# Optimization experiments

Measured on AMD Instinct MI355X. Metric: run time of the kernel, lower is better.

The kernel has to match this reference:

```python
import jax, jax.numpy as jnp
import numpy as np

N_NODES = 50000
N_EDGES = 1_600_000
HIDDEN = 128
BOND = 16


def setup_inputs() -> dict:
    key = jax.random.key(0)
    ks = jax.random.split(key, 6)
    h = jax.random.normal(ks[0], (N_NODES, HIDDEN), dtype=jnp.float32)
    edge_index = jax.random.randint(ks[1], (2, N_EDGES), 0, N_NODES, dtype=jnp.int32)
    bond_features = jax.random.normal(ks[2], (N_EDGES, BOND), dtype=jnp.float32)
    fan_in1 = 2 * HIDDEN + BOND
    W1 = jax.random.normal(ks[3], (fan_in1, HIDDEN), dtype=jnp.float32) / np.sqrt(fan_in1)
    b1 = jnp.zeros((HIDDEN,), dtype=jnp.float32)
    W2 = jax.random.normal(ks[4], (HIDDEN, HIDDEN), dtype=jnp.float32) / np.sqrt(HIDDEN)
    b2 = jnp.zeros((HIDDEN,), dtype=jnp.float32)
    return {"h": h, "edge_index": edge_index, "bond_features": bond_features,
            "W1": W1, "b1": b1, "W2": W2, "b2": b2}


def reference(h, edge_index, bond_features, W1, b1, W2, b2):
    row, col = edge_index[0], edge_index[1]
    # gather endpoint features + bond features -> [E, 2H+B]
    msgs = jnp.concatenate([h[row], h[col], bond_features], axis=-1)
    # 2-layer MLP with SiLU
    msgs = jax.nn.silu(msgs @ W1 + b1) @ W2 + b2  # [E, H]
    # scatter-add back to source nodes (index_add_ on row)
    h_out = jax.ops.segment_sum(msgs, row, num_segments=h.shape[0])
    return h_out
```

## Files before the change

### kernel.cpp

```cpp
#include <hip/hip_runtime.h>

typedef __attribute__((ext_vector_type(4))) float  f32x4;
typedef __attribute__((ext_vector_type(2))) float  f32x2;
typedef __attribute__((ext_vector_type(8))) short  s16x8;
typedef __attribute__((ext_vector_type(4))) float  f4v;
typedef __attribute__((ext_vector_type(4))) int    i32x4;

#define MFMA_BF16 __builtin_amdgcn_mfma_f32_16x16x32_bf16
#define SENT 0x7fffffff

#if defined(__has_builtin)
#if __has_builtin(__builtin_amdgcn_cvt_pk_fp8_f32) && __has_builtin(__builtin_amdgcn_cvt_pk_f32_fp8)
#define HW8 1
#endif
#endif

__device__ __forceinline__ short f2bf(float f) {
  unsigned u = __builtin_bit_cast(unsigned, f);
  u += 0x7fffu + ((u >> 16) & 1u);
  return (short)(u >> 16);
}
__device__ __forceinline__ float bf2f(short s) {
  unsigned u = ((unsigned)(unsigned short)s) << 16;
  return __builtin_bit_cast(float, u);
}
__device__ __forceinline__ s16x8 cvt8(f4v f0, f4v f1) {
  s16x8 r;
  r[0] = f2bf(f0[0]); r[1] = f2bf(f0[1]); r[2] = f2bf(f0[2]); r[3] = f2bf(f0[3]);
  r[4] = f2bf(f1[0]); r[5] = f2bf(f1[1]); r[6] = f2bf(f1[2]); r[7] = f2bf(f1[3]);
  return r;
}
__device__ __forceinline__ unsigned cvtpk_bf16(float a, float b) {
  unsigned r;
  asm("v_cvt_pk_bf16_f32 %0, %1, %2" : "=v"(r) : "v"(a), "v"(b));
  return r;
}
__device__ __forceinline__ unsigned f2fp8(float x) {
  unsigned u = __builtin_bit_cast(unsigned, x);
  unsigned s = (u >> 24) & 0x80u;
  unsigned au = u & 0x7fffffffu;
  if (au < 0x3C800000u) return s;
  unsigned biased = au - 0x3C000000u;
  unsigned val = biased >> 20;
  unsigned rem = biased & 0xFFFFFu;
  val += (rem > 0x80000u) || (rem == 0x80000u && (val & 1u));
  if (val > 0x7Eu) val = 0x7Eu;
  return s | val;
}
__device__ __forceinline__ float fp8tof(unsigned b) {
  unsigned em = b & 0x7fu;
  unsigned f = ((em + 960u) << 20) | ((b & 0x80u) << 24);
  return (em < 8u) ? 0.f : __builtin_bit_cast(float, f);
}
__device__ __forceinline__ unsigned char enc_fp8(float x) {
#ifdef HW8
  return (unsigned char)(__builtin_amdgcn_cvt_pk_fp8_f32(x, x, 0u, false) & 0xffu);
#else
  return (unsigned char)f2fp8(x);
#endif
}
__device__ __forceinline__ void dec_fp8x4(unsigned d, float* f) {
#ifdef HW8
  f32x2 lo = __builtin_amdgcn_cvt_pk_f32_fp8(d, false);
  f32x2 hi = __builtin_amdgcn_cvt_pk_f32_fp8(d, true);
  f[0] = lo[0]; f[1] = lo[1]; f[2] = hi[0]; f[3] = hi[1];
#else
#pragma unroll
  for (int j = 0; j < 4; ++j) f[j] = fp8tof((d >> (8 * j)) & 0xffu);
#endif
}

__global__ __launch_bounds__(256) void prep_weights(
    const float* __restrict__ W1, const float* __restrict__ W2,
    short* __restrict__ wp, float* __restrict__ out, int outN4,
    int* __restrict__ cnt, int NN) {
  int t = blockIdx.x * 256 + threadIdx.x;
  int total = gridDim.x * 256;
  if (out) {
    f32x4* o4 = reinterpret_cast<f32x4*>(out);
    for (int i = t; i < outN4; i += total) o4[i] = (f32x4){0.f, 0.f, 0.f, 0.f};
  }
  if (cnt) {
    for (int i = t; i < NN; i += total) cnt[i] = 0;
  }
  int chunk = t >> 6, l = t & 63;
  if (chunk >= 104) return;
  int q = l >> 4, c = l & 15;
  s16x8 v;
  if (chunk < 72) {
    int kk = chunk >> 3, nt = chunk & 7;
    int k0 = kk * 32 + q * 8, n = nt * 16 + c;
#pragma unroll
    for (int j = 0; j < 8; ++j) {
      int k = k0 + j;
      v[j] = (k < 272) ? f2bf(W1[k * 128 + n]) : (short)0;
    }
    *reinterpret_cast<s16x8*>(wp + (size_t)chunk * 512 + l * 8) = v;
  } else {
    int c2 = chunk - 72;
    int kk = c2 >> 3, nt = c2 & 7;
    int k0 = kk * 32 + q * 8, n = nt * 16 + c;
#pragma unroll
    for (int j = 0; j < 8; ++j) v[j] = f2bf(W2[(k0 + j) * 128 + n]);
    *reinterpret_cast<s16x8*>(wp + 36864 + (size_t)c2 * 512 + l * 8) = v;
  }
}

#define NB_H 512
__global__ __launch_bounds__(256) void k_gh(
    const float* __restrict__ h, const short* __restrict__ wp,
    short* __restrict__ Gs, const int* __restrict__ ei,
    int* __restrict__ cnt, int NN, int NB_G, int E) {
  if ((int)blockIdx.x >= NB_G) {
    int i = ((int)blockIdx.x - NB_G) * 256 + threadIdx.x;
    for (; i < E; i += NB_H * 256) atomicAdd(&cnt[ei[i]], 1);
    return;
  }
  const int tid = threadIdx.x;
  const int w = tid >> 6, l = tid & 63;
  const int q = l >> 4, c = l & 15;
  const int nb = blockIdx.x * 64 + w * 16;

  f32x4 acc[16];
#pragma unroll
  for (int nt = 0; nt < 16; ++nt) acc[nt] = (f32x4){0.f, 0.f, 0.f, 0.f};

#pragma unroll
  for (int kk = 0; kk < 4; ++kk) {
    int node = nb + c; if (node >= NN) node = NN - 1;
    const float* src = h + (size_t)node * 128 + kk * 32 + q * 8;
    s16x8 a = cvt8(*reinterpret_cast<const f4v*>(src),
                   *reinterpret_cast<const f4v*>(src + 4));
#pragma unroll
    for (int nt2 = 0; nt2 < 16; ++nt2) {
      int kkg = kk + ((nt2 >= 8) ? 4 : 0);
      int chunk = kkg * 8 + (nt2 & 7);
      s16x8 b = *reinterpret_cast<const s16x8*>(wp + (size_t)chunk * 512 + l * 8);
      acc[nt2] = MFMA_BF16(a, b, acc[nt2], 0, 0, 0);
    }
  }
  unsigned char* Gb = (unsigned char*)Gs;
#pragma unroll
  for (int nt2 = 0; nt2 < 16; ++nt2)
#pragma unroll
    for (int r = 0; r < 4; ++r) {
      int node = nb + q * 4 + r;
      if (node < NN) {
        if (nt2 < 8) {
          Gs[(size_t)node * 192 + nt2 * 16 + c] = f2bf(acc[nt2][r]);
        } else {
          int n7 = nt2 - 8;
          int addr = ((n7 & 1) * 2 + (c >> 3)) * 32 + (n7 >> 1) * 8 + (c & 7);
          Gb[(size_t)node * 384 + 256 + addr] = enc_fp8(acc[nt2][r]);
        }
      }
    }
}

__global__ __launch_bounds__(1024) void k_s1(const int* __restrict__ cnt,
                                             int* __restrict__ partial, int NN) {
  __shared__ int red[16];
  int t = threadIdx.x, idx = blockIdx.x * 1024 + t;
  int v = (idx < NN) ? cnt[idx] : 0;
#pragma unroll
  for (int d = 1; d < 64; d <<= 1) v += __shfl_xor(v, d);
  if ((t & 63) == 0) red[t >> 6] = v;
  __syncthreads();
  if (t == 0) {
    int s = 0;
#pragma unroll
    for (int i = 0; i < 16; ++i) s += red[i];
    partial[blockIdx.x] = s;
  }
}
__global__ __launch_bounds__(1024) void k_s2(int* __restrict__ partial, int P) {
  __shared__ int ps[1024];
  int t = threadIdx.x;
  int v = (t < P) ? partial[t] : 0;
  ps[t] = v; __syncthreads();
  for (int d = 1; d < 1024; d <<= 1) {
    int u = (t >= d) ? ps[t - d] : 0;
    __syncthreads(); ps[t] += u; __syncthreads();
  }
  if (t < P) partial[t] = ps[t] - v;
}
__global__ __launch_bounds__(1024) void k_s3(int* __restrict__ cnt,
                                             const int* __restrict__ partial, int NN) {
  __shared__ int ps[1024];
  int t = threadIdx.x, idx = blockIdx.x * 1024 + t;
  int v = (idx < NN) ? cnt[idx] : 0;
  ps[t] = v; __syncthreads();
  for (int d = 1; d < 1024; d <<= 1) {
    int u = (t >= d) ? ps[t - d] : 0;
    __syncthreads(); ps[t] += u; __syncthreads();
  }
  if (idx < NN) cnt[idx] = ps[t] - v + partial[blockIdx.x];
}

__global__ void k_scatter8(const int* __restrict__ ei, int* __restrict__ cnt,
                           int* __restrict__ rc, short* __restrict__ bond_s,
                           const float* __restrict__ bond, int E) {
  int i = blockIdx.x * blockDim.x + threadIdx.x;
  int stride = gridDim.x * blockDim.x;
  for (; i < E; i += stride) {
    int r = ei[i], c = ei[(size_t)E + i];
    int pos = atomicAdd(&cnt[r], 1);
    rc[pos] = r | (c << 16);
    const f4v* b4 = reinterpret_cast<const f4v*>(bond + (size_t)i * 16);
    s16x8 lo = cvt8(b4[0], b4[1]);
    s16x8 hi = cvt8(b4[2], b4[3]);
    s16x8* dst = reinterpret_cast<s16x8*>(bond_s + (size_t)pos * 16);
    dst[0] = lo;
    dst[1] = hi;
  }
}

__global__ __launch_bounds__(256, 6) void edge_mlp12(
    const short* __restrict__ Gs, const int* __restrict__ rc,
    const short* __restrict__ bond_s, const short* __restrict__ wp,
    const float* __restrict__ b1, const float* __restrict__ b2,
    float* __restrict__ out, int E) {
  __shared__ __align__(16) char ubuf[4 * 16 * 136 * 2];
  short (*Plds)[16][136] = reinterpret_cast<short(*)[16][136]>(ubuf);
  float (*Sred)[16][68]  = reinterpret_cast<float(*)[16][68]>(ubuf);

  const int tid = threadIdx.x;
  const int w = tid >> 6, l = tid & 63;
  const int q = l >> 4, c = l & 15;

  int nwg = gridDim.x;
  int qq = nwg >> 3, rr = nwg & 7;
  int xcd = blockIdx.x & 7, idx = blockIdx.x >> 3;
  int sbid = (xcd < rr ? xcd * (qq + 1) : rr * (qq + 1) + (xcd - rr) * qq) + idx;
  const int eb = sbid * 64;
  const int we = w * 16;

  int rcv = 0xFFFF;
  if (l < 16) {
    int gpos = eb + we + l;
    if (gpos < E) rcv = rc[gpos];
  }
  int v = __shfl(rcv, c);
  int rv = v & 0xffff;
  int rA = (rv == 0xFFFF) ? 0 : rv;
  int cA = ((unsigned)v) >> 16;

  int vn = __shfl(rcv, (l + 1) & 63);
  unsigned long long bm = __ballot(
      (l < 16) && ((rcv & 0xffff) != ((l < 15) ? (vn & 0xffff) : -1)));

  s16x8 g1v[4];
  i32x4 g2v[2];
  s16x8 az = {};
  {
    const short* gb = Gs + (size_t)rA * 192;
#pragma unroll
    for (int kk = 0; kk < 4; ++kk)
      g1v[kk] = *reinterpret_cast<const s16x8*>(gb + kk * 32 + q * 8);
    const char* g2b = (const char*)Gs + (size_t)cA * 384 + 256 + q * 32;
    g2v[0] = *reinterpret_cast<const i32x4*>(g2b);
    g2v[1] = *reinterpret_cast<const i32x4*>(g2b + 16);
    if (q < 2) {
      int ge = eb + we + c; if (ge >= E) ge = E - 1;
      az = *reinterpret_cast<const s16x8*>(bond_s + (size_t)ge * 16 + q * 8);
    }
  }

  f32x4 acc[8];
#pragma unroll
  for (int nt = 0; nt < 8; ++nt) acc[nt] = (f32x4){0.f, 0.f, 0.f, 0.f};
#pragma unroll
  for (int nt = 0; nt < 8; ++nt) {
    s16x8 b = *reinterpret_cast<const s16x8*>(wp + (size_t)(64 + nt) * 512 + l * 8);
    acc[nt] = MFMA_BF16(az, b, acc[nt], 0, 0, 0);
  }

#pragma unroll
  for (int nt = 0; nt < 8; ++nt) {
    float bias = b1[nt * 16 + c];
    unsigned p01 = cvtpk_bf16(acc[nt][0] + bias, acc[nt][1] + bias);
    unsigned p23 = cvtpk_bf16(acc[nt][2] + bias, acc[nt][3] + bias);
    Plds[w][q * 4 + 0][nt * 16 + c] = (short)(p01 & 0xffffu);
    Plds[w][q * 4 + 1][nt * 16 + c] = (short)(p01 >> 16);
    Plds[w][q * 4 + 2][nt * 16 + c] = (short)(p23 & 0xffffu);
    Plds[w][q * 4 + 3][nt * 16 + c] = (short)(p23 >> 16);
  }

#pragma unroll
  for (int nt = 0; nt < 8; ++nt) acc[nt] = (f32x4){0.f, 0.f, 0.f, 0.f};

#pragma unroll
  for (int kk = 0; kk < 4; ++kk) {
    s16x8 gk = g1v[kk];
    unsigned d0 = (unsigned)g2v[kk >> 1][(kk & 1) * 2 + 0];
    unsigned d1 = (unsigned)g2v[kk >> 1][(kk & 1) * 2 + 1];
    float g2f[8];
    dec_fp8x4(d0, g2f);
    dec_fp8x4(d1, g2f + 4);
    s16x8 pb = *reinterpret_cast<const s16x8*>(&Plds[w][c][kk * 32 + q * 8]);
    float sv[8];
#pragma unroll
    for (int j = 0; j < 8; ++j) {
      float x = bf2f(gk[j]) + g2f[j] + bf2f(pb[j]);
      float e = __expf(-x);
      sv[j] = x * __builtin_amdgcn_rcpf(1.f + e);
    }
    i32x4 a2w;
#pragma unroll
    for (int p = 0; p < 4; ++p)
      a2w[p] = (int)cvtpk_bf16(sv[2 * p], sv[2 * p + 1]);
    s16x8 a2 = __builtin_bit_cast(s16x8, a2w);
#pragma unroll
    for (int nt = 0; nt < 8; ++nt) {
      s16x8 b = *reinterpret_cast<const s16x8*>(wp + 36864 + (size_t)(kk * 8 + nt) * 512 + l * 8);
      acc[nt] = MFMA_BF16(a2, b, acc[nt], 0, 0, 0);
    }
  }

#pragma unroll
  for (int h2 = 0; h2 < 2; ++h2) {
#pragma unroll
    for (int nt2 = 0; nt2 < 4; ++nt2) {
      int nt = h2 * 4 + nt2;
      float bias = b2[nt * 16 + c];
#pragma unroll
      for (int r = 0; r < 4; ++r)
        Sred[w][q * 4 + r][nt2 * 16 + c] = acc[nt][r] + bias;
    }
    float vsum = 0.f;
#pragma unroll
    for (int r = 0; r < 16; ++r) {
      vsum += Sred[w][r][l];
      if ((bm >> r) & 1ull) {
        int rowv = __shfl(rcv, r) & 0xffff;
        if (rowv != 0xFFFF)
          unsafeAtomicAdd(&out[(size_t)rowv * 128 + h2 * 64 + l], vsum);
        vsum = 0.f;
      }
    }
  }
}

__global__ __launch_bounds__(256, 2) void edge_mlp(
    const float* __restrict__ h, const int* __restrict__ ei,
    const float* __restrict__ bond, const short* __restrict__ wp,
    const float* __restrict__ b1, const float* __restrict__ b2,
    float* __restrict__ out, int E) {
  __shared__ __align__(16) short Plds[4][64][136];
  __shared__ int rows_s[256];
  __shared__ int cols_s[256];
  const int tid = threadIdx.x;
  const int w = tid >> 6, l = tid & 63;
  const int q = l >> 4, c = l & 15;
  const int eb = blockIdx.x * 256;
  {
    int e = eb + tid; if (e >= E) e = E - 1;
    rows_s[tid] = ei[e];
    cols_s[tid] = ei[(size_t)E + e];
  }
  __syncthreads();
  const int we = w * 64;
  int rN[4], cN[4], eI[4];
#pragma unroll
  for (int mi = 0; mi < 4; ++mi) {
    int el = we + mi * 16 + c;
    rN[mi] = rows_s[el]; cN[mi] = cols_s[el];
    int eg = eb + el; if (eg >= E) eg = E - 1;
    eI[mi] = eg;
  }
  f32x4 acc[4][8];
#pragma unroll
  for (int mi = 0; mi < 4; ++mi)
#pragma unroll
    for (int nt = 0; nt < 8; ++nt) acc[mi][nt] = (f32x4){0.f, 0.f, 0.f, 0.f};
#pragma unroll
  for (int part = 0; part < 2; ++part) {
#pragma unroll
    for (int kk = 0; kk < 4; ++kk) {
      s16x8 a[4];
#pragma unroll
      for (int mi = 0; mi < 4; ++mi) {
        int node = part ? cN[mi] : rN[mi];
        const float* src = h + (size_t)node * 128 + kk * 32 + q * 8;
        a[mi] = cvt8(*reinterpret_cast<const f4v*>(src),
                     *reinterpret_cast<const f4v*>(src + 4));
      }
      const int kkg = part * 4 + kk;
#pragma unroll
      for (int nt = 0; nt < 8; ++nt) {
        s16x8 b = *reinterpret_cast<const s16x8*>(wp + (size_t)(kkg * 8 + nt) * 512 + l * 8);
#pragma unroll
        for (int mi = 0; mi < 4; ++mi)
          acc[mi][nt] = MFMA_BF16(a[mi], b, acc[mi][nt], 0, 0, 0);
      }
    }
  }
  {
    s16x8 a[4];
#pragma unroll
    for (int mi = 0; mi < 4; ++mi) {
      s16x8 az = {};
      if (q < 2) {
        const float* src = bond + (size_t)eI[mi] * 16 + q * 8;
        az = cvt8(*reinterpret_cast<const f4v*>(src),
                  *reinterpret_cast<const f4v*>(src + 4));
      }
      a[mi] = az;
    }
#pragma unroll
    for (int nt = 0; nt < 8; ++nt) {
      s16x8 b = *reinterpret_cast<const s16x8*>(wp + (size_t)(64 + nt) * 512 + l * 8);
#pragma unroll
      for (int mi = 0; mi < 4; ++mi)
        acc[mi][nt] = MFMA_BF16(a[mi], b, acc[mi][nt], 0, 0, 0);
    }
  }
#pragma unroll
  for (int nt = 0; nt < 8; ++nt) {
    float bias = b1[nt * 16 + c];
#pragma unroll
    for (int mi = 0; mi < 4; ++mi)
#pragma unroll
      for (int r = 0; r < 4; ++r) {
        float x = acc[mi][nt][r] + bias;
        float s = x / (1.f + __expf(-x));
        Plds[w][mi * 16 + q * 4 + r][nt * 16 + c] = f2bf(s);
      }
  }
  f32x4 acc2[4][8];
#pragma unroll
  for (int mi = 0; mi < 4; ++mi)
#pragma unroll
    for (int nt = 0; nt < 8; ++nt) acc2[mi][nt] = (f32x4){0.f, 0.f, 0.f, 0.f};
#pragma unroll
  for (int kk = 0; kk < 4; ++kk) {
    s16x8 a2[4];
#pragma unroll
    for (int mi = 0; mi < 4; ++mi)
      a2[mi] = *reinterpret_cast<const s16x8*>(&Plds[w][mi * 16 + c][kk * 32 + q * 8]);
#pragma unroll
    for (int nt = 0; nt < 8; ++nt) {
      s16x8 b = *reinterpret_cast<const s16x8*>(wp + 36864 + (size_t)(kk * 8 + nt) * 512 + l * 8);
#pragma unroll
      for (int mi = 0; mi < 4; ++mi)
        acc2[mi][nt] = MFMA_BF16(a2[mi], b, acc2[mi][nt], 0, 0, 0);
    }
  }
#pragma unroll
  for (int nt = 0; nt < 8; ++nt) {
    float bias = b2[nt * 16 + c];
#pragma unroll
    for (int mi = 0; mi < 4; ++mi)
#pragma unroll
      for (int r = 0; r < 4; ++r) {
        int el = we + mi * 16 + q * 4 + r;
        if ((eb + el) < E) {
          int node = rows_s[el];
          unsafeAtomicAdd(&out[(size_t)node * 128 + nt * 16 + c],
                          acc2[mi][nt][r] + bias);
        }
      }
  }
}

extern "C" void kernel_launch(void* const* d_in, const int* in_sizes, int n_in,
                              void* d_out, int out_size, void* d_ws, size_t ws_size,
                              hipStream_t stream) {
  const float* h    = (const float*)d_in[0];
  const int*   ei   = (const int*)d_in[1];
  const float* bond = (const float*)d_in[2];
  const float* W1   = (const float*)d_in[3];
  const float* b1   = (const float*)d_in[4];
  const float* W2   = (const float*)d_in[5];
  const float* b2   = (const float*)d_in[6];
  float* out = (float*)d_out;
  char* ws = (char*)d_ws;

  const int E  = in_sizes[1] / 2;
  const int NN = in_sizes[0] / 128;

  short* wp = (short*)ws;
  size_t off_G    = 131072;
  size_t off_cnt  = off_G + (size_t)NN * 384;
  size_t off_par  = off_cnt + (((size_t)NN * 4 + 15) & ~15ull);
  size_t off_idx  = off_par + 4096;
  size_t off_bs   = off_idx + (((size_t)E * 4 + 15) & ~15ull);
  size_t need12   = off_bs + (size_t)E * 32;

  if (ws_size >= need12 && NN <= 65535) {
    short* Gs     = (short*)(ws + off_G);
    int*   cnt    = (int*)(ws + off_cnt);
    int*   par    = (int*)(ws + off_par);
    int*   rc     = (int*)(ws + off_idx);
    short* bond_s = (short*)(ws + off_bs);
    const int NB_G = (NN + 63) / 64;
    const int P    = (NN + 1023) / 1024;

    prep_weights<<<512, 256, 0, stream>>>(W1, W2, wp, out, NN * 32, cnt, NN);
    k_gh<<<NB_G + NB_H, 256, 0, stream>>>(h, wp, Gs, ei, cnt, NN, NB_G, E);
    k_s1<<<P, 1024, 0, stream>>>(cnt, par, NN);
    k_s2<<<1, 1024, 0, stream>>>(par, P);
    k_s3<<<P, 1024, 0, stream>>>(cnt, par, NN);
    k_scatter8<<<2048, 256, 0, stream>>>(ei, cnt, rc, bond_s, bond, E);
    edge_mlp12<<<(E + 63) / 64, 256, 0, stream>>>(Gs, rc, bond_s, wp, b1, b2, out, E);
  } else {
    hipMemsetAsync(d_out, 0, (size_t)NN * 128 * sizeof(float), stream);
    prep_weights<<<512, 256, 0, stream>>>(W1, W2, wp, (float*)nullptr, 0,
                                          (int*)nullptr, 0);
    edge_mlp<<<(E + 255) / 256, 256, 0, stream>>>(h, ei, bond, wp, b1, b2, out, E);
  }
}
```

Measured before the change: 438.8 us.

## Store sorted bond features as fp8, merge scan kernels, prioritize MFMA waves

The staged bond features are now stored as fp8 (16 bytes per edge instead of 32 in bf16) by the scatter kernel. The MLP kernel decodes them back to bf16 before the MFMA, which halves the write and read traffic for that buffer. The separate single-block partial-scan kernel is folded into the final scan kernel: each block sums the preceding partials itself, removing one launch. s_setprio is raised around the MFMA loops to favor matrix issue. The fp8 bond inputs lose precision, and the merged scan assumes at most 64 partial blocks.

```diff
diff --git a/kernel.cpp b/kernel.cpp
--- a/kernel.cpp
+++ b/kernel.cpp
@@ -59,6 +59,15 @@
   return (unsigned char)f2fp8(x);
 #endif
 }
+__device__ __forceinline__ unsigned enc_fp8x4(f4v v) {
+#ifdef HW8
+  unsigned u = __builtin_amdgcn_cvt_pk_fp8_f32(v[0], v[1], 0u, false);
+  u = __builtin_amdgcn_cvt_pk_fp8_f32(v[2], v[3], u, true);
+  return u;
+#else
+  return f2fp8(v[0]) | (f2fp8(v[1]) << 8) | (f2fp8(v[2]) << 16) | (f2fp8(v[3]) << 24);
+#endif
+}
 __device__ __forceinline__ void dec_fp8x4(unsigned d, float* f) {
 #ifdef HW8
   f32x2 lo = __builtin_amdgcn_cvt_pk_f32_fp8(d, false);
@@ -173,33 +182,33 @@
     partial[blockIdx.x] = s;
   }
 }
-__global__ __launch_bounds__(1024) void k_s2(int* __restrict__ partial, int P) {
+__global__ __launch_bounds__(1024) void k_s3m(int* __restrict__ cnt,
+                                              const int* __restrict__ partial,
+                                              int NN) {
   __shared__ int ps[1024];
-  int t = threadIdx.x;
-  int v = (t < P) ? partial[t] : 0;
-  ps[t] = v; __syncthreads();
+  __shared__ int pbuf[64];
+  __shared__ int base_s;
+  int t = threadIdx.x, bid = blockIdx.x, idx = bid * 1024 + t;
+  if (t < 64) pbuf[t] = (t < bid) ? partial[t] : 0;
+  int v = (idx < NN) ? cnt[idx] : 0;
+  ps[t] = v;
+  __syncthreads();
+  if (t == 0) {
+    int b = 0;
+#pragma unroll
+    for (int j = 0; j < 64; ++j) b += pbuf[j];
+    base_s = b;
+  }
   for (int d = 1; d < 1024; d <<= 1) {
     int u = (t >= d) ? ps[t - d] : 0;
     __syncthreads(); ps[t] += u; __syncthreads();
   }
-  if (t < P) partial[t] = ps[t] - v;
-}
-__global__ __launch_bounds__(1024) void k_s3(int* __restrict__ cnt,
-                                             const int* __restrict__ partial, int NN) {
-  __shared__ int ps[1024];
-  int t = threadIdx.x, idx = blockIdx.x * 1024 + t;
-  int v = (idx < NN) ? cnt[idx] : 0;
-  ps[t] = v; __syncthreads();
-  for (int d = 1; d < 1024; d <<= 1) {
-    int u = (t >= d) ? ps[t - d] : 0;
-    __syncthreads(); ps[t] += u; __syncthreads();
-  }
-  if (idx < NN) cnt[idx] = ps[t] - v + partial[blockIdx.x];
-}
-
-__global__ void k_scatter8(const int* __restrict__ ei, int* __restrict__ cnt,
-                           int* __restrict__ rc, short* __restrict__ bond_s,
-                           const float* __restrict__ bond, int E) {
+  if (idx < NN) cnt[idx] = ps[t] - v + base_s;
+}
+
+__global__ void k_scatter13(const int* __restrict__ ei, int* __restrict__ cnt,
+                            int* __restrict__ rc, unsigned* __restrict__ bond8,
+                            const float* __restrict__ bond, int E) {
   int i = blockIdx.x * blockDim.x + threadIdx.x;
   int stride = gridDim.x * blockDim.x;
   for (; i < E; i += stride) {
@@ -207,17 +216,18 @@
     int pos = atomicAdd(&cnt[r], 1);
     rc[pos] = r | (c << 16);
     const f4v* b4 = reinterpret_cast<const f4v*>(bond + (size_t)i * 16);
-    s16x8 lo = cvt8(b4[0], b4[1]);
-    s16x8 hi = cvt8(b4[2], b4[3]);
-    s16x8* dst = reinterpret_cast<s16x8*>(bond_s + (size_t)pos * 16);
-    dst[0] = lo;
-    dst[1] = hi;
-  }
-}
-
-__global__ __launch_bounds__(256, 6) void edge_mlp12(
+    i32x4 o;
+    o[0] = (int)enc_fp8x4(b4[0]);
+    o[1] = (int)enc_fp8x4(b4[1]);
+    o[2] = (int)enc_fp8x4(b4[2]);
+    o[3] = (int)enc_fp8x4(b4[3]);
+    *reinterpret_cast<i32x4*>(bond8 + (size_t)pos * 4) = o;
+  }
+}
+
+__global__ __launch_bounds__(256, 6) void edge_mlp13(
     const short* __restrict__ Gs, const int* __restrict__ rc,
-    const short* __restrict__ bond_s, const short* __restrict__ wp,
+    const unsigned* __restrict__ bond8, const short* __restrict__ wp,
     const float* __restrict__ b1, const float* __restrict__ b2,
     float* __restrict__ out, int E) {
   __shared__ __align__(16) char ubuf[4 * 16 * 136 * 2];
@@ -262,18 +272,28 @@
     g2v[1] = *reinterpret_cast<const i32x4*>(g2b + 16);
     if (q < 2) {
       int ge = eb + we + c; if (ge >= E) ge = E - 1;
-      az = *reinterpret_cast<const s16x8*>(bond_s + (size_t)ge * 16 + q * 8);
+      uint2 d = *reinterpret_cast<const uint2*>(bond8 + (size_t)ge * 4 + q * 2);
+      float f[8];
+      dec_fp8x4(d.x, f);
+      dec_fp8x4(d.y, f + 4);
+      i32x4 aw;
+#pragma unroll
+      for (int p = 0; p < 4; ++p)
+        aw[p] = (int)cvtpk_bf16(f[2 * p], f[2 * p + 1]);
+      az = __builtin_bit_cast(s16x8, aw);
     }
   }
 
   f32x4 acc[8];
 #pragma unroll
   for (int nt = 0; nt < 8; ++nt) acc[nt] = (f32x4){0.f, 0.f, 0.f, 0.f};
+  __builtin_amdgcn_s_setprio(1);
 #pragma unroll
   for (int nt = 0; nt < 8; ++nt) {
     s16x8 b = *reinterpret_cast<const s16x8*>(wp + (size_t)(64 + nt) * 512 + l * 8);
     acc[nt] = MFMA_BF16(az, b, acc[nt], 0, 0, 0);
   }
+  __builtin_amdgcn_s_setprio(0);
 
 #pragma unroll
   for (int nt = 0; nt < 8; ++nt) {
@@ -310,11 +330,13 @@
     for (int p = 0; p < 4; ++p)
       a2w[p] = (int)cvtpk_bf16(sv[2 * p], sv[2 * p + 1]);
     s16x8 a2 = __builtin_bit_cast(s16x8, a2w);
+    __builtin_amdgcn_s_setprio(1);
 #pragma unroll
     for (int nt = 0; nt < 8; ++nt) {
       s16x8 b = *reinterpret_cast<const s16x8*>(wp + 36864 + (size_t)(kk * 8 + nt) * 512 + l * 8);
       acc[nt] = MFMA_BF16(a2, b, acc[nt], 0, 0, 0);
     }
+    __builtin_amdgcn_s_setprio(0);
   }
 
 #pragma unroll
@@ -485,24 +507,23 @@
   size_t off_par  = off_cnt + (((size_t)NN * 4 + 15) & ~15ull);
   size_t off_idx  = off_par + 4096;
   size_t off_bs   = off_idx + (((size_t)E * 4 + 15) & ~15ull);
-  size_t need12   = off_bs + (size_t)E * 32;
-
-  if (ws_size >= need12 && NN <= 65535) {
-    short* Gs     = (short*)(ws + off_G);
-    int*   cnt    = (int*)(ws + off_cnt);
-    int*   par    = (int*)(ws + off_par);
-    int*   rc     = (int*)(ws + off_idx);
-    short* bond_s = (short*)(ws + off_bs);
+  size_t need13   = off_bs + (size_t)E * 16;
+
+  if (ws_size >= need13 && NN <= 65535) {
+    short*    Gs    = (short*)(ws + off_G);
+    int*      cnt   = (int*)(ws + off_cnt);
+    int*      par   = (int*)(ws + off_par);
+    int*      rc    = (int*)(ws + off_idx);
+    unsigned* bond8 = (unsigned*)(ws + off_bs);
     const int NB_G = (NN + 63) / 64;
     const int P    = (NN + 1023) / 1024;
 
     prep_weights<<<512, 256, 0, stream>>>(W1, W2, wp, out, NN * 32, cnt, NN);
     k_gh<<<NB_G + NB_H, 256, 0, stream>>>(h, wp, Gs, ei, cnt, NN, NB_G, E);
     k_s1<<<P, 1024, 0, stream>>>(cnt, par, NN);
-    k_s2<<<1, 1024, 0, stream>>>(par, P);
-    k_s3<<<P, 1024, 0, stream>>>(cnt, par, NN);
-    k_scatter8<<<2048, 256, 0, stream>>>(ei, cnt, rc, bond_s, bond, E);
-    edge_mlp12<<<(E + 63) / 64, 256, 0, stream>>>(Gs, rc, bond_s, wp, b1, b2, out, E);
+    k_s3m<<<P, 1024, 0, stream>>>(cnt, par, NN);
+    k_scatter13<<<2048, 256, 0, stream>>>(ei, cnt, rc, bond8, bond, E);
+    edge_mlp13<<<(E + 63) / 64, 256, 0, stream>>>(Gs, rc, bond8, wp, b1, b2, out, E);
   } else {
     hipMemsetAsync(d_out, 0, (size_t)NN * 128 * sizeof(float), stream);
     prep_weights<<<512, 256, 0, stream>>>(W1, W2, wp, (float*)nullptr, 0,
```

After: 393.4 us. 10.4% less time.
